# Kernel optimization log

Measured on AMD Instinct MI355X. Metric: run time of the kernel, lower is better.

Reference implementation:

```python
import jax, jax.numpy as jnp
import numpy as np

B, S, H = 2, 1024, 2048
NH, HD = 16, 128
L = 4  # num_prev_layers == attention_window


def _rope(x):
    # x: [..., S, D]; standard rotate-half RoPE, base 10000
    d = x.shape[-1]
    s = x.shape[-2]
    inv_freq = 1.0 / (10000.0 ** (jnp.arange(0, d, 2, dtype=jnp.float32) / d))
    freqs = jnp.outer(jnp.arange(s, dtype=jnp.float32), inv_freq)  # [S, d/2]
    cos, sin = jnp.cos(freqs), jnp.sin(freqs)
    x1, x2 = jnp.split(x, 2, axis=-1)
    return jnp.concatenate([x1 * cos - x2 * sin, x2 * cos + x1 * sin], axis=-1)


def setup_inputs() -> dict:
    key = jax.random.key(0)
    ks = jax.random.split(key, 8)
    std = 0.02
    return {
        "hidden_states": jax.random.normal(ks[0], (B, S, H), jnp.float32),
        "prev_hidden_states": jax.random.normal(ks[1], (L, B, S, H), jnp.float32),
        "Wq": jax.random.normal(ks[2], (H, NH * HD), jnp.float32) * std,
        "bq": jnp.zeros((NH * HD,), jnp.float32),
        "Wk": jax.random.normal(ks[3], (H, NH * HD), jnp.float32) * std,
        "bk": jnp.zeros((NH * HD,), jnp.float32),
        "Wv": jax.random.normal(ks[4], (H, NH * HD), jnp.float32) * std,
        "bv": jnp.zeros((NH * HD,), jnp.float32),
        "Wo": jax.random.normal(ks[5], (NH * HD, H), jnp.float32) * std,
        "bo": jnp.zeros((H,), jnp.float32),
        "Wg": jax.random.normal(ks[6], (H, L), jnp.float32) * std,
    }


def reference(hidden_states, prev_hidden_states, Wq, bq, Wk, bk, Wv, bv, Wo, bo, Wg):
    b, s, _ = hidden_states.shape
    # queries from current layer: [b, nh, s, hd], RoPE applied
    q = (hidden_states @ Wq + bq).reshape(b, s, NH, HD).transpose(0, 2, 1, 3)
    q = _rope(q)
    # keys/values from each prev layer: [L, b, nh, s, hd]
    k = (prev_hidden_states @ Wk + bk).reshape(L, b, s, NH, HD).transpose(0, 1, 3, 2, 4)
    k = _rope(k)
    v = (prev_hidden_states @ Wv + bv).reshape(L, b, s, NH, HD).transpose(0, 1, 3, 2, 4)
    # per-prev-layer attention (no mask)
    scores = jnp.einsum('bhqd,lbhkd->lbhqk', q, k) / jnp.sqrt(jnp.float32(HD))
    attn = jax.nn.softmax(scores, axis=-1)
    lo = jnp.einsum('lbhqk,lbhkd->lbhqd', attn, v)
    lo = lo.transpose(0, 1, 3, 2, 4).reshape(L, b, s, NH * HD)  # merge heads
    # softmax gate over pooled queries -> combine layer outputs
    layer_w = jax.nn.softmax(jnp.mean(hidden_states, axis=1) @ Wg, axis=-1)  # [b, L]
    out = jnp.einsum('lbsh,bl->bsh', lo, layer_w)
    return out @ Wo + bo
```

## Files before the change

kernel.cpp:

```cpp
#include <hip/hip_runtime.h>
#include <hip/hip_bf16.h>
#include <math.h>


typedef __bf16 bf16;
typedef __bf16 bf16x4v __attribute__((ext_vector_type(4)));
typedef __bf16 bf16x8 __attribute__((ext_vector_type(8)));
typedef float f32x4 __attribute__((ext_vector_type(4)));

#define DEV static __device__ __forceinline__

DEV void gload_lds16(const void* g, void* s) {
  __builtin_amdgcn_global_load_lds(
      (const __attribute__((address_space(1))) void*)g,
      (__attribute__((address_space(3))) void*)s, 16, 0, 0);
}

DEV f32x4 mfma16(bf16x8 a, bf16x8 b, f32x4 c) {
  return __builtin_amdgcn_mfma_f32_16x16x32_bf16(a, b, c, 0, 0, 0);
}

__global__ __launch_bounds__(256) void cvt_kernel(const float* __restrict__ in,
                                                  bf16* __restrict__ out, int n4) {
  int i = blockIdx.x * 256 + threadIdx.x;
  if (i >= n4) return;
  const float4 v = ((const float4*)in)[i];
  bf16x4v o;
  o.x = (bf16)v.x; o.y = (bf16)v.y; o.z = (bf16)v.z; o.w = (bf16)v.w;
  ((bf16x4v*)out)[i] = o;
}

__global__ __launch_bounds__(256) void twt4_kernel(
    const float* __restrict__ W0, const float* __restrict__ W1,
    const float* __restrict__ W2, const float* __restrict__ W3,
    bf16* __restrict__ T0, bf16* __restrict__ T1, bf16* __restrict__ T2,
    bf16* __restrict__ T3) {
  const float* W = (blockIdx.z == 0) ? W0 : (blockIdx.z == 1) ? W1
                    : (blockIdx.z == 2) ? W2 : W3;
  bf16* Wt = (blockIdx.z == 0) ? T0 : (blockIdx.z == 1) ? T1
              : (blockIdx.z == 2) ? T2 : T3;
  __shared__ float tile[64][65];
  const int t = threadIdx.x;
  const int n0 = blockIdx.x * 64, k0 = blockIdx.y * 64;
#pragma unroll
  for (int ph = 0; ph < 16; ++ph) {
    int idx = ph * 256 + t, r = idx >> 6, c = idx & 63;
    tile[r][c] = W[(size_t)(k0 + r) * 2048 + n0 + c];
  }
  __syncthreads();
#pragma unroll
  for (int ph = 0; ph < 16; ++ph) {
    int idx = ph * 256 + t, r = idx >> 6, c = idx & 63;
    Wt[(size_t)(n0 + r) * 2048 + k0 + c] = (bf16)tile[c][r];
  }
}

__global__ __launch_bounds__(64) void rope_table_kernel(float* __restrict__ cosT,
                                                        float* __restrict__ sinT) {
  int s = blockIdx.x, j = threadIdx.x;
  float inv = powf(10000.0f, -(float)j * (1.0f / 64.0f));
  float a = (float)s * inv;
  cosT[s * 64 + j] = cosf(a);
  sinT[s * 64 + j] = sinf(a);
}

__global__ __launch_bounds__(256) void mean_part_kernel(const float* __restrict__ hs,
                                                        float* __restrict__ part) {
  int bc = blockIdx.x;
  int b = bc >> 3, c0 = (bc & 7) * 256;
  int ss = blockIdx.y;
  int col = c0 + threadIdx.x;
  float s = 0.f;
  for (int r = 0; r < 128; ++r)
    s += hs[((size_t)b * 1024 + ss * 128 + r) * 2048 + col];
  part[(size_t)ss * 4096 + b * 2048 + col] = s;
}

__global__ __launch_bounds__(256) void mean_fin_kernel(const float* __restrict__ part,
                                                       float* __restrict__ meanb) {
  int c = blockIdx.x * 256 + threadIdx.x;
  float s = 0.f;
#pragma unroll
  for (int j = 0; j < 8; ++j) s += part[(size_t)j * 4096 + c];
  meanb[c] = s * (1.0f / 1024.0f);
}

__global__ __launch_bounds__(256) void gate_kernel(const float* __restrict__ meanb,
                                                   const float* __restrict__ Wg,
                                                   float* __restrict__ lwout) {
  __shared__ float red[8][256];
  int t = threadIdx.x;
  float p[8];
#pragma unroll
  for (int j = 0; j < 8; ++j) p[j] = 0.f;
  for (int hh = t; hh < 2048; hh += 256) {
    float m0 = meanb[hh], m1 = meanb[2048 + hh];
#pragma unroll
    for (int ll = 0; ll < 4; ++ll) {
      float g = Wg[hh * 4 + ll];
      p[ll] += m0 * g;
      p[4 + ll] += m1 * g;
    }
  }
#pragma unroll
  for (int j = 0; j < 8; ++j) red[j][t] = p[j];
  __syncthreads();
  for (int s2 = 128; s2 > 0; s2 >>= 1) {
    if (t < s2) {
#pragma unroll
      for (int j = 0; j < 8; ++j) red[j][t] += red[j][t + s2];
    }
    __syncthreads();
  }
  if (t == 0) {
#pragma unroll
    for (int bb = 0; bb < 2; ++bb) {
      float v0 = red[bb * 4 + 0][0], v1 = red[bb * 4 + 1][0];
      float v2 = red[bb * 4 + 2][0], v3 = red[bb * 4 + 3][0];
      float mx = fmaxf(fmaxf(v0, v1), fmaxf(v2, v3));
      float e0 = __expf(v0 - mx), e1 = __expf(v1 - mx);
      float e2 = __expf(v2 - mx), e3 = __expf(v3 - mx);
      float inv = 1.0f / (e0 + e1 + e2 + e3);
      lwout[bb * 4 + 0] = e0 * inv;
      lwout[bb * 4 + 1] = e1 * inv;
      lwout[bb * 4 + 2] = e2 * inv;
      lwout[bb * 4 + 3] = e3 * inv;
    }
  }
}

template <int OUTMODE>
__global__ __launch_bounds__(256) void gemm_kernel(const bf16* __restrict__ A,
                                                   const bf16* __restrict__ Bt,
                                                   const float* __restrict__ bias,
                                                   void* __restrict__ Cout,
                                                   int M, int N, int K,
                                                   const float* __restrict__ cosT,
                                                   const float* __restrict__ sinT) {
  __shared__ __attribute__((aligned(16))) bf16 As[2][128 * 64];
  __shared__ __attribute__((aligned(16))) bf16 Bs[2][128 * 64];
  const int t = threadIdx.x;
  const int w = t >> 6, l = t & 63;
  const int lo = l & 15, hi = l >> 4;
  const int wr = w >> 1, wc = w & 1;

  const int nwg = gridDim.x * gridDim.y;
  int flat = blockIdx.y * gridDim.x + blockIdx.x;
  int swz = (flat & 7) * (nwg >> 3) + (flat >> 3);
  const int bx = swz % gridDim.x, by = swz / gridDim.x;

  f32x4 acc[4][4];
#pragma unroll
  for (int m = 0; m < 4; ++m)
#pragma unroll
    for (int n = 0; n < 4; ++n)
#pragma unroll
      for (int q = 0; q < 4; ++q) acc[m][n][q] = 0.f;

  int srow[4], scl[4], srowB[4];
#pragma unroll
  for (int p = 0; p < 4; ++p) {
    int id = p * 256 + t;
    int r = id >> 3, cph = id & 7;
    srow[p] = r;
    scl[p] = cph ^ (r & 7);
    srowB[p] = r;
    if (OUTMODE == 4) {
      int a = r >> 5, rr = r & 31;
      srowB[p] = (a == 0) ? rr : (a == 1) ? rr + 64 : (a == 2) ? rr + 32 : rr + 96;
    }
  }

  const bf16* Ab = A + (size_t)by * 128 * K;
  const bf16* Bb = Bt + (size_t)bx * 128 * K;

  auto stage = [&](int bi, int kt) {
#pragma unroll
    for (int p = 0; p < 4; ++p)
      gload_lds16(Ab + (size_t)srow[p] * K + kt + scl[p] * 8,
                  &As[bi][(p * 256 + w * 64) * 8]);
#pragma unroll
    for (int p = 0; p < 4; ++p)
      gload_lds16(Bb + (size_t)srowB[p] * K + kt + scl[p] * 8,
                  &Bs[bi][(p * 256 + w * 64) * 8]);
  };

  stage(0, 0);
  int cur = 0;
  for (int kt = 0; kt < K; kt += 64) {
    if (kt + 64 < K) {
      stage(cur ^ 1, kt + 64);
      asm volatile("s_waitcnt vmcnt(8)" ::: "memory");
    } else {
      asm volatile("s_waitcnt vmcnt(0)" ::: "memory");
    }
    __builtin_amdgcn_s_barrier();
    __builtin_amdgcn_sched_barrier(0);
    __builtin_amdgcn_s_setprio(1);
#pragma unroll
    for (int ks = 0; ks < 2; ++ks) {
      bf16x8 af[4], bfr[4];
#pragma unroll
      for (int m = 0; m < 4; ++m) {
        int row = wr * 64 + m * 16 + lo;
        int ch = (ks * 4 + hi) ^ (row & 7);
        af[m] = *(const bf16x8*)&As[cur][row * 64 + ch * 8];
      }
#pragma unroll
      for (int n = 0; n < 4; ++n) {
        int row = wc * 64 + n * 16 + lo;
        int ch = (ks * 4 + hi) ^ (row & 7);
        bfr[n] = *(const bf16x8*)&Bs[cur][row * 64 + ch * 8];
      }
#pragma unroll
      for (int m = 0; m < 4; ++m)
#pragma unroll
        for (int n = 0; n < 4; ++n)
          acc[m][n] = mfma16(af[m], bfr[n], acc[m][n]);
    }
    __builtin_amdgcn_s_setprio(0);
    __builtin_amdgcn_s_barrier();
    cur ^= 1;
  }

  if (OUTMODE == 4) {
    const int jb = wc * 32;
#pragma unroll
    for (int n = 0; n < 2; ++n) {
      int j = jb + n * 16 + lo;
      float bb1 = bias[bx * 128 + j];
      float bb2 = bias[bx * 128 + j + 64];
#pragma unroll
      for (int m = 0; m < 4; ++m) {
#pragma unroll
        for (int i = 0; i < 4; ++i) {
          size_t row = (size_t)by * 128 + wr * 64 + m * 16 + hi * 4 + i;
          int s_idx = (int)(row & 1023);
          size_t g = (row >> 10) * 16 + bx;
          float x1 = acc[m][n][i] + bb1;
          float x2 = acc[m][n + 2][i] + bb2;
          float cc = cosT[s_idx * 64 + j];
          float ss = sinT[s_idx * 64 + j];
          bf16* dst = (bf16*)Cout + (g * 1024 + s_idx) * 128;
          dst[j] = (bf16)(x1 * cc - x2 * ss);
          dst[j + 64] = (bf16)(x2 * cc + x1 * ss);
        }
      }
    }
  } else {
#pragma unroll
    for (int n = 0; n < 4; ++n) {
      int col = bx * 128 + wc * 64 + n * 16 + lo;
      float bb = bias[col];
#pragma unroll
      for (int m = 0; m < 4; ++m) {
#pragma unroll
        for (int i = 0; i < 4; ++i) {
          size_t row = (size_t)by * 128 + wr * 64 + m * 16 + hi * 4 + i;
          float v = acc[m][n][i] + bb;
          ((float*)Cout)[row * N + col] = v;
        }
      }
    }
  }
}

__global__ __launch_bounds__(512, 2) void gemm_kv_kernel(
    const bf16* __restrict__ prev, const bf16* __restrict__ WkT,
    const bf16* __restrict__ WvT, const float* __restrict__ bk,
    const float* __restrict__ bv, const float* __restrict__ cosT,
    const float* __restrict__ sinT, bf16* __restrict__ Kout,
    bf16* __restrict__ Vout) {
  __shared__ __attribute__((aligned(16))) bf16 As[2][16384];
  __shared__ __attribute__((aligned(16))) bf16 Bs[2][16384];
  const int t = threadIdx.x;
  const int w = t >> 6, l = t & 63;
  const int lo = l & 15, hi = l >> 4;
  const int wm = w >> 2, wn = w & 3;

  const int bid = blockIdx.x;
  const int grp = bid >> 8;
  const int sub = bid & 255;
  const int swz = (sub & 7) * 32 + (sub >> 3);
  const int mt = (grp == 0) ? (swz >> 3) : (swz & 7);
  const int nt = (grp == 0) ? (swz & 7) : (swz >> 3);
  const bf16* Ab = ((grp == 0) ? prev : WvT) + (size_t)mt * 256 * 2048;
  const bf16* Bb = ((grp == 0) ? WkT : prev) + (size_t)nt * 256 * 2048;

  const int r0 = t >> 2;
  const int c8 = ((t & 3) ^ ((r0 >> 1) & 3)) * 8;
  int r0B = r0;
  if (grp == 0) {
    int a = r0 >> 5, rr = r0 & 31;
    r0B = (a == 0) ? rr : (a == 1) ? rr + 64 : (a == 2) ? rr + 32 : rr + 96;
  }

  f32x4 acc[8][4];
#pragma unroll
  for (int m = 0; m < 8; ++m)
#pragma unroll
    for (int n = 0; n < 4; ++n)
#pragma unroll
      for (int q = 0; q < 4; ++q) acc[m][n][q] = 0.f;

  auto gA = [&](int bi, int kh, int p, int koff) {
    gload_lds16(Ab + (size_t)(p * 128 + r0) * 2048 + koff + kh * 32 + c8,
                &As[bi][kh * 8192 + p * 4096 + w * 512]);
  };
  auto gB = [&](int bi, int kh, int p, int koff) {
    gload_lds16(Bb + (size_t)(p * 128 + r0B) * 2048 + koff + kh * 32 + c8,
                &Bs[bi][kh * 8192 + p * 4096 + w * 512]);
  };

  gA(0, 0, 0, 0); gA(0, 0, 1, 0);
  gB(0, 0, 0, 0); gB(0, 0, 1, 0);
  gA(0, 1, 0, 0); gA(0, 1, 1, 0);
  gB(0, 1, 0, 0); gB(0, 1, 1, 0);
  asm volatile("s_waitcnt vmcnt(4)" ::: "memory");
  __builtin_amdgcn_s_barrier();

  int cur = 0;
  for (int kt = 0; kt < 32; ++kt) {
    const int nxt = cur ^ 1;
    const int koff = (kt + 1) * 64;
    const bool pf = kt < 31;
    bf16x8 af[8], bfr[2];

#pragma unroll
    for (int m = 0; m < 8; ++m) {
      int row = wm * 128 + m * 16 + lo;
      int slot = hi ^ ((row >> 1) & 3);
      af[m] = *(const bf16x8*)&As[cur][row * 32 + slot * 8];
    }
#pragma unroll
    for (int n = 0; n < 2; ++n) {
      int row = wn * 64 + n * 16 + lo;
      int slot = hi ^ ((row >> 1) & 3);
      bfr[n] = *(const bf16x8*)&Bs[cur][row * 32 + slot * 8];
    }
    if (pf) { gA(nxt, 0, 0, koff); gA(nxt, 0, 1, koff); }
    __builtin_amdgcn_s_barrier();
    __builtin_amdgcn_s_setprio(1);
#pragma unroll
    for (int m = 0; m < 8; ++m) {
      acc[m][0] = mfma16(af[m], bfr[0], acc[m][0]);
      acc[m][1] = mfma16(af[m], bfr[1], acc[m][1]);
    }
    __builtin_amdgcn_s_setprio(0);
    __builtin_amdgcn_s_barrier();

#pragma unroll
    for (int n = 0; n < 2; ++n) {
      int row = wn * 64 + (n + 2) * 16 + lo;
      int slot = hi ^ ((row >> 1) & 3);
      bfr[n] = *(const bf16x8*)&Bs[cur][row * 32 + slot * 8];
    }
    if (pf) {
      gB(nxt, 0, 0, koff); gB(nxt, 0, 1, koff);
      asm volatile("s_waitcnt vmcnt(4)" ::: "memory");
    } else {
      asm volatile("s_waitcnt vmcnt(0)" ::: "memory");
    }
    __builtin_amdgcn_s_barrier();
    __builtin_amdgcn_s_setprio(1);
#pragma unroll
    for (int m = 0; m < 8; ++m) {
      acc[m][2] = mfma16(af[m], bfr[0], acc[m][2]);
      acc[m][3] = mfma16(af[m], bfr[1], acc[m][3]);
    }
    __builtin_amdgcn_s_setprio(0);
    __builtin_amdgcn_s_barrier();

#pragma unroll
    for (int m = 0; m < 8; ++m) {
      int row = wm * 128 + m * 16 + lo;
      int slot = hi ^ ((row >> 1) & 3);
      af[m] = *(const bf16x8*)&As[cur][8192 + row * 32 + slot * 8];
    }
#pragma unroll
    for (int n = 0; n < 2; ++n) {
      int row = wn * 64 + n * 16 + lo;
      int slot = hi ^ ((row >> 1) & 3);
      bfr[n] = *(const bf16x8*)&Bs[cur][8192 + row * 32 + slot * 8];
    }
    if (pf) { gA(nxt, 1, 0, koff); gA(nxt, 1, 1, koff); }
    __builtin_amdgcn_s_barrier();
    __builtin_amdgcn_s_setprio(1);
#pragma unroll
    for (int m = 0; m < 8; ++m) {
      acc[m][0] = mfma16(af[m], bfr[0], acc[m][0]);
      acc[m][1] = mfma16(af[m], bfr[1], acc[m][1]);
    }
    __builtin_amdgcn_s_setprio(0);
    __builtin_amdgcn_s_barrier();

#pragma unroll
    for (int n = 0; n < 2; ++n) {
      int row = wn * 64 + (n + 2) * 16 + lo;
      int slot = hi ^ ((row >> 1) & 3);
      bfr[n] = *(const bf16x8*)&Bs[cur][8192 + row * 32 + slot * 8];
    }
    if (pf) {
      gB(nxt, 1, 0, koff); gB(nxt, 1, 1, koff);
      asm volatile("s_waitcnt vmcnt(4)" ::: "memory");
    } else {
      asm volatile("s_waitcnt vmcnt(0)" ::: "memory");
    }
    __builtin_amdgcn_s_barrier();
    __builtin_amdgcn_s_setprio(1);
#pragma unroll
    for (int m = 0; m < 8; ++m) {
      acc[m][2] = mfma16(af[m], bfr[0], acc[m][2]);
      acc[m][3] = mfma16(af[m], bfr[1], acc[m][3]);
    }
    __builtin_amdgcn_s_setprio(0);
    __builtin_amdgcn_s_barrier();

    cur = nxt;
  }

  if (grp == 0) {
    const int headg = nt * 2 + (wn >> 1);
    const int jbase = (wn & 1) * 32;
#pragma unroll
    for (int n = 0; n < 2; ++n) {
      int j = jbase + n * 16 + lo;
      float bb1 = bk[headg * 128 + j];
      float bb2 = bk[headg * 128 + j + 64];
#pragma unroll
      for (int m = 0; m < 8; ++m) {
#pragma unroll
        for (int i = 0; i < 4; ++i) {
          size_t srow = (size_t)mt * 256 + wm * 128 + m * 16 + hi * 4 + i;
          int s_idx = (int)(srow & 1023);
          size_t g = (srow >> 10) * 16 + headg;
          float x1 = acc[m][n][i] + bb1;
          float x2 = acc[m][n + 2][i] + bb2;
          float cc = cosT[s_idx * 64 + j];
          float ss = sinT[s_idx * 64 + j];
          bf16* dst = Kout + (g * 1024 + s_idx) * 128;
          dst[j] = (bf16)(x1 * cc - x2 * ss);
          dst[j + 64] = (bf16)(x2 * cc + x1 * ss);
        }
      }
    }
  } else {
#pragma unroll
    for (int m = 0; m < 8; ++m) {
#pragma unroll
      for (int i = 0; i < 4; ++i) {
        size_t row = (size_t)mt * 256 + wm * 128 + m * 16 + hi * 4 + i;
        float rb = bv[row];
#pragma unroll
        for (int n = 0; n < 4; ++n) {
          int col = nt * 256 + wn * 64 + n * 16 + lo;
          int pos64 = ((n >> 1) << 5) + ((lo >> 2) << 3) + ((n & 1) << 2) + (lo & 3);
          int colp = (col & ~63) | pos64;
          float v = acc[m][n][i] + rb;
          Vout[(size_t)(colp >> 10) * 2097152 + row * 1024 + (colp & 1023)] =
              (bf16)v;
        }
      }
    }
  }
}

__global__ __launch_bounds__(256, 2) void attn_kernel(const bf16* __restrict__ Q,
                                                      const bf16* __restrict__ Kb,
                                                      const bf16* __restrict__ Vt,
                                                      const float* __restrict__ lw,
                                                      bf16* __restrict__ Obuf) {
  __shared__ __attribute__((aligned(16))) bf16 Ks[2][64 * 128];
  __shared__ __attribute__((aligned(16))) bf16 Vs[2][128 * 64];
  const int t = threadIdx.x, w = t >> 6, l = t & 63;
  const int lo = l & 15, hi = l >> 4;
  const int bh = blockIdx.x;
  const int qt = blockIdx.y;
  const int li = blockIdx.z;
  const int b = bh >> 4, h = bh & 15;
  const float C2 = 0.08838834764831845f * 1.44269504f;
  const float M2 = 64.0f * C2;
  const bf16 one_ = (bf16)1.0f;
  const bf16x8 ones8 = {one_, one_, one_, one_, one_, one_, one_, one_};

  bf16x8 qf[2][4];
#pragma unroll
  for (int qs = 0; qs < 2; ++qs) {
    const bf16* qptr =
        Q + ((size_t)bh * 1024 + qt * 128 + w * 32 + qs * 16 + lo) * 128;
#pragma unroll
    for (int db = 0; db < 4; ++db)
      qf[qs][db] = *(const bf16x8*)(qptr + db * 32 + hi * 8);
  }

  int krow[4], kcl[4], vrow[4], vcl[4];
#pragma unroll
  for (int p = 0; p < 4; ++p) {
    int id = p * 256 + t;
    krow[p] = id >> 4;
    kcl[p] = (id & 15) ^ (krow[p] & 7);
    vrow[p] = id >> 3;
    vcl[p] = (id & 7) ^ (vrow[p] & 7);
  }

  const bf16* Kl = Kb + ((size_t)li * 32 + bh) * (size_t)131072;
  const bf16* Vl = Vt + ((size_t)li * 32 + bh) * (size_t)131072;

  f32x4 dacc[2];
  f32x4 oacc[2][8];
#pragma unroll
  for (int qs = 0; qs < 2; ++qs) {
#pragma unroll
    for (int q = 0; q < 4; ++q) dacc[qs][q] = 0.f;
#pragma unroll
    for (int dc = 0; dc < 8; ++dc)
#pragma unroll
      for (int q = 0; q < 4; ++q) oacc[qs][dc][q] = 0.f;
  }

  auto stage = [&](int bi, int kt2) {
    const bf16* Ksrc = Kl + (size_t)kt2 * 8192;
#pragma unroll
    for (int p = 0; p < 4; ++p)
      gload_lds16(Ksrc + (size_t)krow[p] * 128 + kcl[p] * 8,
                  &Ks[bi][(p * 256 + w * 64) * 8]);
#pragma unroll
    for (int p = 0; p < 4; ++p)
      gload_lds16(Vl + (size_t)vrow[p] * 1024 + kt2 * 64 + vcl[p] * 8,
                  &Vs[bi][(p * 256 + w * 64) * 8]);
  };

  auto softmax_step = [&](f32x4 (&sa)[4], bf16x8 (&pf2)[2]) {
    bf16x4v pk[4];
#pragma unroll
    for (int kc = 0; kc < 4; ++kc) {
#pragma unroll
      for (int i = 0; i < 4; ++i) {
        float pf_ = __builtin_amdgcn_exp2f(fmaf(sa[kc][i], C2, -M2));
        pk[kc][i] = (bf16)pf_;
      }
    }
    pf2[0] = __builtin_shufflevector(pk[0], pk[1], 0, 1, 2, 3, 4, 5, 6, 7);
    pf2[1] = __builtin_shufflevector(pk[2], pk[3], 0, 1, 2, 3, 4, 5, 6, 7);
  };

  stage(0, 0);
  int cur = 0;
  for (int kt = 0; kt < 16; ++kt) {
    if (kt < 15) {
      stage(cur ^ 1, kt + 1);
      asm volatile("s_waitcnt vmcnt(8)" ::: "memory");
    } else {
      asm volatile("s_waitcnt vmcnt(0)" ::: "memory");
    }
    __builtin_amdgcn_s_barrier();
    __builtin_amdgcn_sched_barrier(0);

    f32x4 sa[2][4];
#pragma unroll
    for (int qs = 0; qs < 2; ++qs)
#pragma unroll
      for (int kc = 0; kc < 4; ++kc)
#pragma unroll
        for (int q = 0; q < 4; ++q) sa[qs][kc][q] = 0.f;
    __builtin_amdgcn_s_setprio(1);
#pragma unroll
    for (int kc = 0; kc < 4; ++kc) {
      int row = kc * 16 + lo;
#pragma unroll
      for (int db = 0; db < 4; ++db) {
        int ch = (db * 4 + hi) ^ (row & 7);
        bf16x8 kf = *(const bf16x8*)&Ks[cur][row * 128 + ch * 8];
        sa[0][kc] = mfma16(kf, qf[0][db], sa[0][kc]);
        sa[1][kc] = mfma16(kf, qf[1][db], sa[1][kc]);
      }
    }
    __builtin_amdgcn_s_setprio(0);

    bf16x8 pfr[2][2];
    softmax_step(sa[0], pfr[0]);
    softmax_step(sa[1], pfr[1]);

    __builtin_amdgcn_s_setprio(1);
#pragma unroll
    for (int kvc = 0; kvc < 2; ++kvc) {
      dacc[0] = mfma16(pfr[0][kvc], ones8, dacc[0]);
      dacc[1] = mfma16(pfr[1][kvc], ones8, dacc[1]);
#pragma unroll
      for (int dc = 0; dc < 8; ++dc) {
        int rowv = dc * 16 + lo;
        int ch = (kvc * 4 + hi) ^ (rowv & 7);
        bf16x8 vf = *(const bf16x8*)&Vs[cur][rowv * 64 + ch * 8];
        oacc[0][dc] = mfma16(pfr[0][kvc], vf, oacc[0][dc]);
        oacc[1][dc] = mfma16(pfr[1][kvc], vf, oacc[1][dc]);
      }
    }
    __builtin_amdgcn_s_setprio(0);
    __builtin_amdgcn_s_barrier();
    cur ^= 1;
  }

  float wl = lw[b * 4 + li];
#pragma unroll
  for (int qs = 0; qs < 2; ++qs) {
    float inv[4];
#pragma unroll
    for (int i = 0; i < 4; ++i) inv[i] = wl / dacc[qs][i];
#pragma unroll
    for (int dc = 0; dc < 8; ++dc) {
      int col = h * 128 + dc * 16 + lo;
#pragma unroll
      for (int i = 0; i < 4; ++i) {
        int srow = qt * 128 + w * 32 + qs * 16 + hi * 4 + i;
        Obuf[((size_t)(li * 2 + b) * 1024 + srow) * 2048 + col] =
            (bf16)(oacc[qs][dc][i] * inv[i]);
      }
    }
  }
}

__global__ __launch_bounds__(256) void comb_kernel(const bf16* __restrict__ Obuf,
                                                   bf16* __restrict__ comb) {
  size_t i = ((size_t)blockIdx.x * 256 + threadIdx.x) * 8;
  bf16x8 a0 = *(const bf16x8*)(Obuf + i);
  bf16x8 a1 = *(const bf16x8*)(Obuf + 4194304 + i);
  bf16x8 a2 = *(const bf16x8*)(Obuf + 8388608 + i);
  bf16x8 a3 = *(const bf16x8*)(Obuf + 12582912 + i);
  bf16x8 o;
#pragma unroll
  for (int j = 0; j < 8; ++j)
    o[j] = (bf16)((float)a0[j] + (float)a1[j] + (float)a2[j] + (float)a3[j]);
  *(bf16x8*)(comb + i) = o;
}

extern "C" void kernel_launch(void* const* d_in, const int* in_sizes, int n_in,
                              void* d_out, int out_size, void* d_ws, size_t ws_size,
                              hipStream_t stream) {
  (void)in_sizes; (void)n_in; (void)out_size; (void)ws_size;
  const float* hs = (const float*)d_in[0];
  const float* prev = (const float*)d_in[1];
  const float* Wq = (const float*)d_in[2];
  const float* bq = (const float*)d_in[3];
  const float* Wk = (const float*)d_in[4];
  const float* bk = (const float*)d_in[5];
  const float* Wv = (const float*)d_in[6];
  const float* bv = (const float*)d_in[7];
  const float* Wo = (const float*)d_in[8];
  const float* bo = (const float*)d_in[9];
  const float* Wg = (const float*)d_in[10];
  float* out = (float*)d_out;

  char* ws = (char*)d_ws;
  bf16* hs_bf = (bf16*)(ws + 0);
  bf16* prev_bf = (bf16*)(ws + 8388608);
  bf16* WqT = (bf16*)(ws + 41943040);
  bf16* WkT = (bf16*)(ws + 50331648);
  bf16* WvT = (bf16*)(ws + 58720256);
  bf16* Qbf = (bf16*)(ws + 67108864);
  bf16* WoT = (bf16*)(ws + 75497472);
  bf16* Kbf = (bf16*)(ws + 83886080);
  bf16* Vt = (bf16*)(ws + 117440512);
  float* cosT = (float*)(ws + 150994944);
  float* sinT = (float*)(ws + 151257088);
  float* part = (float*)(ws + 151519232);
  float* meanb = (float*)(ws + 151650304);
  float* lwbuf = (float*)(ws + 151666688);
  bf16* Obuf = prev_bf;
  bf16* comb = (bf16*)(ws + 0);

  cvt_kernel<<<4096, 256, 0, stream>>>(hs, hs_bf, 2048 * 2048 / 4);
  cvt_kernel<<<16384, 256, 0, stream>>>(prev, prev_bf, 8192 * 2048 / 4);

  twt4_kernel<<<dim3(32, 32, 4), 256, 0, stream>>>(Wq, Wk, Wv, Wo, WqT, WkT,
                                                   WvT, WoT);

  rope_table_kernel<<<1024, 64, 0, stream>>>(cosT, sinT);
  mean_part_kernel<<<dim3(16, 8), 256, 0, stream>>>(hs, part);
  mean_fin_kernel<<<16, 256, 0, stream>>>(part, meanb);
  gate_kernel<<<1, 256, 0, stream>>>(meanb, Wg, lwbuf);

  gemm_kernel<4><<<dim3(16, 16), 256, 0, stream>>>(hs_bf, WqT, bq, Qbf, 2048,
                                                   2048, 2048, cosT, sinT);
  gemm_kv_kernel<<<512, 512, 0, stream>>>(prev_bf, WkT, WvT, bk, bv, cosT, sinT,
                                          Kbf, Vt);

  attn_kernel<<<dim3(32, 8, 4), 256, 0, stream>>>(Qbf, Kbf, Vt, lwbuf, Obuf);

  comb_kernel<<<2048, 256, 0, stream>>>(Obuf, comb);

  gemm_kernel<1><<<dim3(16, 16), 256, 0, stream>>>(comb, WoT, bo, out, 2048,
                                                   2048, 2048, nullptr, nullptr);
}
```

Measured before the change: 338.3 us.

## Simplify KV GEMM main loop to single-stage BK=32 double-buffered pipeline

The KV projection GEMM's K-step drops from 64 to 32 per iteration (64 iterations instead of 32), and the four interleaved load/compute phases per iteration are replaced by one phase. Each phase issues the next tile's global-to-LDS loads, waits, takes a barrier, then reads all A/B fragments and runs 32 MFMAs. LDS use is halved, which may allow better occupancy. In exchange there are more barriers per unit of work, and less fine-grained overlap between loads and MFMAs.

```diff
diff --git a/kernel.cpp b/kernel.cpp
--- a/kernel.cpp
+++ b/kernel.cpp
@@ -271,8 +271,8 @@
     const float* __restrict__ bv, const float* __restrict__ cosT,
     const float* __restrict__ sinT, bf16* __restrict__ Kout,
     bf16* __restrict__ Vout) {
-  __shared__ __attribute__((aligned(16))) bf16 As[2][16384];
-  __shared__ __attribute__((aligned(16))) bf16 Bs[2][16384];
+  __shared__ __attribute__((aligned(16))) bf16 As[2][8192];
+  __shared__ __attribute__((aligned(16))) bf16 Bs[2][8192];
   const int t = threadIdx.x;
   const int w = t >> 6, l = t & 63;
   const int lo = l & 15, hi = l >> 4;
@@ -303,29 +303,33 @@
 #pragma unroll
       for (int q = 0; q < 4; ++q) acc[m][n][q] = 0.f;
 
-  auto gA = [&](int bi, int kh, int p, int koff) {
-    gload_lds16(Ab + (size_t)(p * 128 + r0) * 2048 + koff + kh * 32 + c8,
-                &As[bi][kh * 8192 + p * 4096 + w * 512]);
+  auto gA = [&](int bi, int p, int koff) {
+    gload_lds16(Ab + (size_t)(p * 128 + r0) * 2048 + koff + c8,
+                &As[bi][p * 4096 + w * 512]);
   };
-  auto gB = [&](int bi, int kh, int p, int koff) {
-    gload_lds16(Bb + (size_t)(p * 128 + r0B) * 2048 + koff + kh * 32 + c8,
-                &Bs[bi][kh * 8192 + p * 4096 + w * 512]);
+  auto gB = [&](int bi, int p, int koff) {
+    gload_lds16(Bb + (size_t)(p * 128 + r0B) * 2048 + koff + c8,
+                &Bs[bi][p * 4096 + w * 512]);
   };
 
-  gA(0, 0, 0, 0); gA(0, 0, 1, 0);
-  gB(0, 0, 0, 0); gB(0, 0, 1, 0);
-  gA(0, 1, 0, 0); gA(0, 1, 1, 0);
-  gB(0, 1, 0, 0); gB(0, 1, 1, 0);
-  asm volatile("s_waitcnt vmcnt(4)" ::: "memory");
-  __builtin_amdgcn_s_barrier();
+  gA(0, 0, 0); gA(0, 1, 0);
+  gB(0, 0, 0); gB(0, 1, 0);
 
   int cur = 0;
-  for (int kt = 0; kt < 32; ++kt) {
+  for (int kt = 0; kt < 64; ++kt) {
     const int nxt = cur ^ 1;
-    const int koff = (kt + 1) * 64;
-    const bool pf = kt < 31;
-    bf16x8 af[8], bfr[2];
-
+    const int koff = (kt + 1) * 32;
+    if (kt < 63) {
+      gA(nxt, 0, koff); gA(nxt, 1, koff);
+      gB(nxt, 0, koff); gB(nxt, 1, koff);
+      asm volatile("s_waitcnt vmcnt(4)" ::: "memory");
+    } else {
+      asm volatile("s_waitcnt vmcnt(0)" ::: "memory");
+    }
+    __builtin_amdgcn_s_barrier();
+    __builtin_amdgcn_sched_barrier(0);
+
+    bf16x8 af[8], bfr[4];
 #pragma unroll
     for (int m = 0; m < 8; ++m) {
       int row = wm * 128 + m * 16 + lo;
@@ -333,89 +337,19 @@
       af[m] = *(const bf16x8*)&As[cur][row * 32 + slot * 8];
     }
 #pragma unroll
-    for (int n = 0; n < 2; ++n) {
+    for (int n = 0; n < 4; ++n) {
       int row = wn * 64 + n * 16 + lo;
       int slot = hi ^ ((row >> 1) & 3);
       bfr[n] = *(const bf16x8*)&Bs[cur][row * 32 + slot * 8];
     }
-    if (pf) { gA(nxt, 0, 0, koff); gA(nxt, 0, 1, koff); }
-    __builtin_amdgcn_s_barrier();
     __builtin_amdgcn_s_setprio(1);
 #pragma unroll
-    for (int m = 0; m < 8; ++m) {
-      acc[m][0] = mfma16(af[m], bfr[0], acc[m][0]);
-      acc[m][1] = mfma16(af[m], bfr[1], acc[m][1]);
-    }
+    for (int m = 0; m < 8; ++m)
+#pragma unroll
+      for (int n = 0; n < 4; ++n)
+        acc[m][n] = mfma16(af[m], bfr[n], acc[m][n]);
     __builtin_amdgcn_s_setprio(0);
     __builtin_amdgcn_s_barrier();
-
-#pragma unroll
-    for (int n = 0; n < 2; ++n) {
-      int row = wn * 64 + (n + 2) * 16 + lo;
-      int slot = hi ^ ((row >> 1) & 3);
-      bfr[n] = *(const bf16x8*)&Bs[cur][row * 32 + slot * 8];
-    }
-    if (pf) {
-      gB(nxt, 0, 0, koff); gB(nxt, 0, 1, koff);
-      asm volatile("s_waitcnt vmcnt(4)" ::: "memory");
-    } else {
-      asm volatile("s_waitcnt vmcnt(0)" ::: "memory");
-    }
-    __builtin_amdgcn_s_barrier();
-    __builtin_amdgcn_s_setprio(1);
-#pragma unroll
-    for (int m = 0; m < 8; ++m) {
-      acc[m][2] = mfma16(af[m], bfr[0], acc[m][2]);
-      acc[m][3] = mfma16(af[m], bfr[1], acc[m][3]);
-    }
-    __builtin_amdgcn_s_setprio(0);
-    __builtin_amdgcn_s_barrier();
-
-#pragma unroll
-    for (int m = 0; m < 8; ++m) {
-      int row = wm * 128 + m * 16 + lo;
-      int slot = hi ^ ((row >> 1) & 3);
-      af[m] = *(const bf16x8*)&As[cur][8192 + row * 32 + slot * 8];
-    }
-#pragma unroll
-    for (int n = 0; n < 2; ++n) {
-      int row = wn * 64 + n * 16 + lo;
-      int slot = hi ^ ((row >> 1) & 3);
-      bfr[n] = *(const bf16x8*)&Bs[cur][8192 + row * 32 + slot * 8];
-    }
-    if (pf) { gA(nxt, 1, 0, koff); gA(nxt, 1, 1, koff); }
-    __builtin_amdgcn_s_barrier();
-    __builtin_amdgcn_s_setprio(1);
-#pragma unroll
-    for (int m = 0; m < 8; ++m) {
-      acc[m][0] = mfma16(af[m], bfr[0], acc[m][0]);
-      acc[m][1] = mfma16(af[m], bfr[1], acc[m][1]);
-    }
-    __builtin_amdgcn_s_setprio(0);
-    __builtin_amdgcn_s_barrier();
-
-#pragma unroll
-    for (int n = 0; n < 2; ++n) {
-      int row = wn * 64 + (n + 2) * 16 + lo;
-      int slot = hi ^ ((row >> 1) & 3);
-      bfr[n] = *(const bf16x8*)&Bs[cur][8192 + row * 32 + slot * 8];
-    }
-    if (pf) {
-      gB(nxt, 1, 0, koff); gB(nxt, 1, 1, koff);
-      asm volatile("s_waitcnt vmcnt(4)" ::: "memory");
-    } else {
-      asm volatile("s_waitcnt vmcnt(0)" ::: "memory");
-    }
-    __builtin_amdgcn_s_barrier();
-    __builtin_amdgcn_s_setprio(1);
-#pragma unroll
-    for (int m = 0; m < 8; ++m) {
-      acc[m][2] = mfma16(af[m], bfr[0], acc[m][2]);
-      acc[m][3] = mfma16(af[m], bfr[1], acc[m][3]);
-    }
-    __builtin_amdgcn_s_setprio(0);
-    __builtin_amdgcn_s_barrier();
-
     cur = nxt;
   }
 
```

Result: slower. 370.9 us (+9.6%).

## Fuse layer-combine into output GEMM A-load and merge small setup kernels

Applied to the files above, without the earlier changes.

The output projection GEMM now reads the four per-layer attention outputs directly, sums them in registers and writes the combined bf16 tile into LDS, removing the separate combine kernel and its intermediate buffer. The RoPE table computation is folded into the weight-transpose launch as an extra z-slice, and the mean finalisation is folded into the gate kernel. This saves launches and a full read/write pass over the combined activations. The cost is that each GEMM tile re-reads four A sources through registers rather than direct-to-LDS loads, which raises L2 traffic and register pressure.

```diff
diff --git a/kernel.cpp b/kernel.cpp
--- a/kernel.cpp
+++ b/kernel.cpp
@@ -30,11 +30,22 @@
   ((bf16x4v*)out)[i] = o;
 }
 
-__global__ __launch_bounds__(256) void twt4_kernel(
+__global__ __launch_bounds__(256) void twt5_kernel(
     const float* __restrict__ W0, const float* __restrict__ W1,
     const float* __restrict__ W2, const float* __restrict__ W3,
     bf16* __restrict__ T0, bf16* __restrict__ T1, bf16* __restrict__ T2,
-    bf16* __restrict__ T3) {
+    bf16* __restrict__ T3, float* __restrict__ cosT, float* __restrict__ sinT) {
+  if (blockIdx.z == 4) {
+    int s = blockIdx.y * 32 + blockIdx.x;
+    if (threadIdx.x < 64) {
+      int j = threadIdx.x;
+      float inv = powf(10000.0f, -(float)j * (1.0f / 64.0f));
+      float a = (float)s * inv;
+      cosT[s * 64 + j] = cosf(a);
+      sinT[s * 64 + j] = sinf(a);
+    }
+    return;
+  }
   const float* W = (blockIdx.z == 0) ? W0 : (blockIdx.z == 1) ? W1
                     : (blockIdx.z == 2) ? W2 : W3;
   bf16* Wt = (blockIdx.z == 0) ? T0 : (blockIdx.z == 1) ? T1
@@ -53,15 +64,6 @@
     int idx = ph * 256 + t, r = idx >> 6, c = idx & 63;
     Wt[(size_t)(n0 + r) * 2048 + k0 + c] = (bf16)tile[c][r];
   }
-}
-
-__global__ __launch_bounds__(64) void rope_table_kernel(float* __restrict__ cosT,
-                                                        float* __restrict__ sinT) {
-  int s = blockIdx.x, j = threadIdx.x;
-  float inv = powf(10000.0f, -(float)j * (1.0f / 64.0f));
-  float a = (float)s * inv;
-  cosT[s * 64 + j] = cosf(a);
-  sinT[s * 64 + j] = sinf(a);
 }
 
 __global__ __launch_bounds__(256) void mean_part_kernel(const float* __restrict__ hs,
@@ -76,16 +78,7 @@
   part[(size_t)ss * 4096 + b * 2048 + col] = s;
 }
 
-__global__ __launch_bounds__(256) void mean_fin_kernel(const float* __restrict__ part,
-                                                       float* __restrict__ meanb) {
-  int c = blockIdx.x * 256 + threadIdx.x;
-  float s = 0.f;
-#pragma unroll
-  for (int j = 0; j < 8; ++j) s += part[(size_t)j * 4096 + c];
-  meanb[c] = s * (1.0f / 1024.0f);
-}
-
-__global__ __launch_bounds__(256) void gate_kernel(const float* __restrict__ meanb,
+__global__ __launch_bounds__(256) void gate_kernel(const float* __restrict__ part,
                                                    const float* __restrict__ Wg,
                                                    float* __restrict__ lwout) {
   __shared__ float red[8][256];
@@ -94,7 +87,14 @@
 #pragma unroll
   for (int j = 0; j < 8; ++j) p[j] = 0.f;
   for (int hh = t; hh < 2048; hh += 256) {
-    float m0 = meanb[hh], m1 = meanb[2048 + hh];
+    float m0 = 0.f, m1 = 0.f;
+#pragma unroll
+    for (int j = 0; j < 8; ++j) {
+      m0 += part[(size_t)j * 4096 + hh];
+      m1 += part[(size_t)j * 4096 + 2048 + hh];
+    }
+    m0 *= (1.0f / 1024.0f);
+    m1 *= (1.0f / 1024.0f);
 #pragma unroll
     for (int ll = 0; ll < 4; ++ll) {
       float g = Wg[hh * 4 + ll];
@@ -129,14 +129,13 @@
   }
 }
 
-template <int OUTMODE>
-__global__ __launch_bounds__(256) void gemm_kernel(const bf16* __restrict__ A,
-                                                   const bf16* __restrict__ Bt,
-                                                   const float* __restrict__ bias,
-                                                   void* __restrict__ Cout,
-                                                   int M, int N, int K,
-                                                   const float* __restrict__ cosT,
-                                                   const float* __restrict__ sinT) {
+__global__ __launch_bounds__(256) void gemm_q_kernel(const bf16* __restrict__ A,
+                                                     const bf16* __restrict__ Bt,
+                                                     const float* __restrict__ bias,
+                                                     bf16* __restrict__ Cout,
+                                                     const float* __restrict__ cosT,
+                                                     const float* __restrict__ sinT) {
+  const int K = 2048;
   __shared__ __attribute__((aligned(16))) bf16 As[2][128 * 64];
   __shared__ __attribute__((aligned(16))) bf16 Bs[2][128 * 64];
   const int t = threadIdx.x;
@@ -164,11 +163,8 @@
     int r = id >> 3, cph = id & 7;
     srow[p] = r;
     scl[p] = cph ^ (r & 7);
-    srowB[p] = r;
-    if (OUTMODE == 4) {
-      int a = r >> 5, rr = r & 31;
-      srowB[p] = (a == 0) ? rr : (a == 1) ? rr + 64 : (a == 2) ? rr + 32 : rr + 96;
-    }
+    int a = r >> 5, rr = r & 31;
+    srowB[p] = (a == 0) ? rr : (a == 1) ? rr + 64 : (a == 2) ? rr + 32 : rr + 96;
   }
 
   const bf16* Ab = A + (size_t)by * 128 * K;
@@ -223,43 +219,159 @@
     cur ^= 1;
   }
 
-  if (OUTMODE == 4) {
-    const int jb = wc * 32;
-#pragma unroll
-    for (int n = 0; n < 2; ++n) {
-      int j = jb + n * 16 + lo;
-      float bb1 = bias[bx * 128 + j];
-      float bb2 = bias[bx * 128 + j + 64];
+  const int jb = wc * 32;
+#pragma unroll
+  for (int n = 0; n < 2; ++n) {
+    int j = jb + n * 16 + lo;
+    float bb1 = bias[bx * 128 + j];
+    float bb2 = bias[bx * 128 + j + 64];
+#pragma unroll
+    for (int m = 0; m < 4; ++m) {
+#pragma unroll
+      for (int i = 0; i < 4; ++i) {
+        size_t row = (size_t)by * 128 + wr * 64 + m * 16 + hi * 4 + i;
+        int s_idx = (int)(row & 1023);
+        size_t g = (row >> 10) * 16 + bx;
+        float x1 = acc[m][n][i] + bb1;
+        float x2 = acc[m][n + 2][i] + bb2;
+        float cc = cosT[s_idx * 64 + j];
+        float ss = sinT[s_idx * 64 + j];
+        bf16* dst = Cout + (g * 1024 + s_idx) * 128;
+        dst[j] = (bf16)(x1 * cc - x2 * ss);
+        dst[j + 64] = (bf16)(x2 * cc + x1 * ss);
+      }
+    }
+  }
+}
+
+__global__ __launch_bounds__(256) void gemm_o_kernel(const bf16* __restrict__ Obuf,
+                                                     const bf16* __restrict__ Bt,
+                                                     const float* __restrict__ bias,
+                                                     float* __restrict__ out) {
+  const int K = 2048;
+  __shared__ __attribute__((aligned(16))) bf16 As[2][128 * 64];
+  __shared__ __attribute__((aligned(16))) bf16 Bs[2][128 * 64];
+  const int t = threadIdx.x;
+  const int w = t >> 6, l = t & 63;
+  const int lo = l & 15, hi = l >> 4;
+  const int wr = w >> 1, wc = w & 1;
+
+  const int nwg = gridDim.x * gridDim.y;
+  int flat = blockIdx.y * gridDim.x + blockIdx.x;
+  int swz = (flat & 7) * (nwg >> 3) + (flat >> 3);
+  const int bx = swz % gridDim.x, by = swz / gridDim.x;
+
+  f32x4 acc[4][4];
+#pragma unroll
+  for (int m = 0; m < 4; ++m)
+#pragma unroll
+    for (int n = 0; n < 4; ++n)
+#pragma unroll
+      for (int q = 0; q < 4; ++q) acc[m][n][q] = 0.f;
+
+  int srow[4], scl[4];
+  const bf16* ap[4][4];
+#pragma unroll
+  for (int p = 0; p < 4; ++p) {
+    int id = p * 256 + t;
+    int r = id >> 3, cph = id & 7;
+    srow[p] = r;
+    scl[p] = cph ^ (r & 7);
+    size_t grow = (size_t)by * 128 + r;
+#pragma unroll
+    for (int sl = 0; sl < 4; ++sl)
+      ap[p][sl] = Obuf + ((size_t)(sl * 2 + (grow >> 10)) * 1024 + (grow & 1023)) * 2048 +
+                  scl[p] * 8;
+  }
+  const bf16* Bb = Bt + (size_t)bx * 128 * K;
+
+  bf16x8 areg[4][4];
+  auto loadA = [&](int kt) {
+#pragma unroll
+    for (int p = 0; p < 4; ++p)
+#pragma unroll
+      for (int sl = 0; sl < 4; ++sl)
+        areg[p][sl] = *(const bf16x8*)(ap[p][sl] + kt);
+  };
+  auto writeA = [&](int bi) {
+#pragma unroll
+    for (int p = 0; p < 4; ++p) {
+      bf16x8 o;
+#pragma unroll
+      for (int j = 0; j < 8; ++j)
+        o[j] = (bf16)((float)areg[p][0][j] + (float)areg[p][1][j] +
+                      (float)areg[p][2][j] + (float)areg[p][3][j]);
+      *(bf16x8*)&As[bi][(p * 256 + t) * 8] = o;
+    }
+  };
+  auto stageB = [&](int bi, int kt) {
+#pragma unroll
+    for (int p = 0; p < 4; ++p)
+      gload_lds16(Bb + (size_t)srow[p] * K + kt + scl[p] * 8,
+                  &Bs[bi][(p * 256 + w * 64) * 8]);
+  };
+
+  loadA(0);
+  writeA(0);
+  stageB(0, 0);
+  loadA(64);
+  asm volatile("s_waitcnt vmcnt(16)" ::: "memory");
+  asm volatile("s_waitcnt lgkmcnt(0)" ::: "memory");
+  __builtin_amdgcn_s_barrier();
+
+  int cur = 0;
+  for (int kt = 0; kt < K; kt += 64) {
+    const bool pf = kt + 64 < K;
+    const bool pf2 = kt + 128 < K;
+    if (pf) {
+      writeA(cur ^ 1);
+      stageB(cur ^ 1, kt + 64);
+      if (pf2) loadA(kt + 128);
+    }
+    __builtin_amdgcn_s_setprio(1);
+#pragma unroll
+    for (int ks = 0; ks < 2; ++ks) {
+      bf16x8 af[4], bfr[4];
 #pragma unroll
       for (int m = 0; m < 4; ++m) {
-#pragma unroll
-        for (int i = 0; i < 4; ++i) {
-          size_t row = (size_t)by * 128 + wr * 64 + m * 16 + hi * 4 + i;
-          int s_idx = (int)(row & 1023);
-          size_t g = (row >> 10) * 16 + bx;
-          float x1 = acc[m][n][i] + bb1;
-          float x2 = acc[m][n + 2][i] + bb2;
-          float cc = cosT[s_idx * 64 + j];
-          float ss = sinT[s_idx * 64 + j];
-          bf16* dst = (bf16*)Cout + (g * 1024 + s_idx) * 128;
-          dst[j] = (bf16)(x1 * cc - x2 * ss);
-          dst[j + 64] = (bf16)(x2 * cc + x1 * ss);
-        }
-      }
-    }
-  } else {
-#pragma unroll
-    for (int n = 0; n < 4; ++n) {
-      int col = bx * 128 + wc * 64 + n * 16 + lo;
-      float bb = bias[col];
-#pragma unroll
-      for (int m = 0; m < 4; ++m) {
-#pragma unroll
-        for (int i = 0; i < 4; ++i) {
-          size_t row = (size_t)by * 128 + wr * 64 + m * 16 + hi * 4 + i;
-          float v = acc[m][n][i] + bb;
-          ((float*)Cout)[row * N + col] = v;
-        }
+        int row = wr * 64 + m * 16 + lo;
+        int ch = (ks * 4 + hi) ^ (row & 7);
+        af[m] = *(const bf16x8*)&As[cur][row * 64 + ch * 8];
+      }
+#pragma unroll
+      for (int n = 0; n < 4; ++n) {
+        int row = wc * 64 + n * 16 + lo;
+        int ch = (ks * 4 + hi) ^ (row & 7);
+        bfr[n] = *(const bf16x8*)&Bs[cur][row * 64 + ch * 8];
+      }
+#pragma unroll
+      for (int m = 0; m < 4; ++m)
+#pragma unroll
+        for (int n = 0; n < 4; ++n)
+          acc[m][n] = mfma16(af[m], bfr[n], acc[m][n]);
+    }
+    __builtin_amdgcn_s_setprio(0);
+    if (pf) {
+      if (pf2)
+        asm volatile("s_waitcnt vmcnt(16)" ::: "memory");
+      else
+        asm volatile("s_waitcnt vmcnt(0)" ::: "memory");
+      asm volatile("s_waitcnt lgkmcnt(0)" ::: "memory");
+      __builtin_amdgcn_s_barrier();
+      cur ^= 1;
+    }
+  }
+
+#pragma unroll
+  for (int n = 0; n < 4; ++n) {
+    int col = bx * 128 + wc * 64 + n * 16 + lo;
+    float bb = bias[col];
+#pragma unroll
+    for (int m = 0; m < 4; ++m) {
+#pragma unroll
+      for (int i = 0; i < 4; ++i) {
+        size_t row = (size_t)by * 128 + wr * 64 + m * 16 + hi * 4 + i;
+        out[row * 2048 + col] = acc[m][n][i] + bb;
       }
     }
   }
@@ -619,20 +731,6 @@
   }
 }
 
-__global__ __launch_bounds__(256) void comb_kernel(const bf16* __restrict__ Obuf,
-                                                   bf16* __restrict__ comb) {
-  size_t i = ((size_t)blockIdx.x * 256 + threadIdx.x) * 8;
-  bf16x8 a0 = *(const bf16x8*)(Obuf + i);
-  bf16x8 a1 = *(const bf16x8*)(Obuf + 4194304 + i);
-  bf16x8 a2 = *(const bf16x8*)(Obuf + 8388608 + i);
-  bf16x8 a3 = *(const bf16x8*)(Obuf + 12582912 + i);
-  bf16x8 o;
-#pragma unroll
-  for (int j = 0; j < 8; ++j)
-    o[j] = (bf16)((float)a0[j] + (float)a1[j] + (float)a2[j] + (float)a3[j]);
-  *(bf16x8*)(comb + i) = o;
-}
-
 extern "C" void kernel_launch(void* const* d_in, const int* in_sizes, int n_in,
                               void* d_out, int out_size, void* d_ws, size_t ws_size,
                               hipStream_t stream) {
@@ -663,31 +761,23 @@
   float* cosT = (float*)(ws + 150994944);
   float* sinT = (float*)(ws + 151257088);
   float* part = (float*)(ws + 151519232);
-  float* meanb = (float*)(ws + 151650304);
   float* lwbuf = (float*)(ws + 151666688);
   bf16* Obuf = prev_bf;
-  bf16* comb = (bf16*)(ws + 0);
 
   cvt_kernel<<<4096, 256, 0, stream>>>(hs, hs_bf, 2048 * 2048 / 4);
   cvt_kernel<<<16384, 256, 0, stream>>>(prev, prev_bf, 8192 * 2048 / 4);
 
-  twt4_kernel<<<dim3(32, 32, 4), 256, 0, stream>>>(Wq, Wk, Wv, Wo, WqT, WkT,
-                                                   WvT, WoT);
-
-  rope_table_kernel<<<1024, 64, 0, stream>>>(cosT, sinT);
+  twt5_kernel<<<dim3(32, 32, 5), 256, 0, stream>>>(Wq, Wk, Wv, Wo, WqT, WkT,
+                                                   WvT, WoT, cosT, sinT);
+
   mean_part_kernel<<<dim3(16, 8), 256, 0, stream>>>(hs, part);
-  mean_fin_kernel<<<16, 256, 0, stream>>>(part, meanb);
-  gate_kernel<<<1, 256, 0, stream>>>(meanb, Wg, lwbuf);
-
-  gemm_kernel<4><<<dim3(16, 16), 256, 0, stream>>>(hs_bf, WqT, bq, Qbf, 2048,
-                                                   2048, 2048, cosT, sinT);
+  gate_kernel<<<1, 256, 0, stream>>>(part, Wg, lwbuf);
+
+  gemm_q_kernel<<<dim3(16, 16), 256, 0, stream>>>(hs_bf, WqT, bq, Qbf, cosT, sinT);
   gemm_kv_kernel<<<512, 512, 0, stream>>>(prev_bf, WkT, WvT, bk, bv, cosT, sinT,
                                           Kbf, Vt);
 
   attn_kernel<<<dim3(32, 8, 4), 256, 0, stream>>>(Qbf, Kbf, Vt, lwbuf, Obuf);
 
-  comb_kernel<<<2048, 256, 0, stream>>>(Obuf, comb);
-
-  gemm_kernel<1><<<dim3(16, 16), 256, 0, stream>>>(comb, WoT, bo, out, 2048,
-                                                   2048, 2048, nullptr, nullptr);
-}
+  gemm_o_kernel<<<dim3(16, 16), 256, 0, stream>>>(Obuf, WoT, bo, out);
+}
```

Measured after the change: 372.5 us. +10.1%, slower.
